# Kernel tuning notes

Measured on AMD Instinct MI355X. Metric: run time of the kernel, lower is better.

## Reference

```python
import jax, jax.numpy as jnp
import numpy as np

DIM = 1024
D_STATE = 16
D_CONV = 4
EXPAND = 2
D_INNER = DIM * EXPAND
DT_RANK = 64  # ceil(1024/16)
N_EXP = 8
TOP_K = 2
HID = DIM * 2
B, T = 2, 2048
EPS = 1e-5


def setup_inputs() -> dict:
    key = jax.random.key(0)
    ks = jax.random.split(key, 16)
    s = 0.02
    # dt bias init (softplus-inverse of dt in [1e-3, 1e-1]) as in the torch code
    dt_init = jnp.exp(jax.random.uniform(ks[0], (D_INNER,)) * (np.log(0.1) - np.log(0.001)) + np.log(0.001))
    dt_proj_b = dt_init + jnp.log(-jnp.expm1(-dt_init))
    A_log = jnp.broadcast_to(jnp.log(jnp.arange(1, D_STATE + 1, dtype=jnp.float32))[None, :], (D_INNER, D_STATE))
    return {
        "x": jax.random.normal(ks[1], (B, T, DIM), jnp.float32),
        "ssm_state": jnp.zeros((B, D_INNER, D_STATE), jnp.float32),
        "conv_state": jnp.zeros((B, D_INNER, D_CONV - 1), jnp.float32),
        "ln1_s": jnp.ones((DIM,), jnp.float32), "ln1_b": jnp.zeros((DIM,), jnp.float32),
        "ln2_s": jnp.ones((DIM,), jnp.float32), "ln2_b": jnp.zeros((DIM,), jnp.float32),
        "in_proj_w": jax.random.normal(ks[2], (2 * D_INNER, DIM), jnp.float32) * s,
        "conv_w": jax.random.normal(ks[3], (D_INNER, 1, D_CONV), jnp.float32) * 0.2,
        "conv_b": jnp.zeros((D_INNER,), jnp.float32),
        "x_proj_w": jax.random.normal(ks[4], (DT_RANK + 2 * D_STATE, D_INNER), jnp.float32) * s,
        "dt_proj_w": jax.random.normal(ks[5], (D_INNER, DT_RANK), jnp.float32) * s,
        "dt_proj_b": dt_proj_b,
        "A_log": A_log,
        "Dp": jnp.ones((D_INNER,), jnp.float32),
        "out_proj_w": jax.random.normal(ks[6], (DIM, D_INNER), jnp.float32) * s,
        "router_w": jax.random.normal(ks[7], (N_EXP, DIM), jnp.float32) * s,
        "w_gate": jax.random.normal(ks[8], (N_EXP, HID, DIM), jnp.float32) * s,
        "w_up": jax.random.normal(ks[9], (N_EXP, HID, DIM), jnp.float32) * s,
        "w_down": jax.random.normal(ks[10], (N_EXP, DIM, HID), jnp.float32) * s,
    }


def _layernorm(x, scale, bias):
    mu = x.mean(-1, keepdims=True)
    var = ((x - mu) ** 2).mean(-1, keepdims=True)
    return (x - mu) * jax.lax.rsqrt(var + EPS) * scale + bias


def _mamba(xn, ssm_state, conv_state, in_proj_w, conv_w, conv_b, x_proj_w, dt_proj_w, dt_proj_b, A_log, Dp, out_proj_w):
    xz = jnp.einsum("btd,ed->bte", xn, in_proj_w)          # [B,T,2*di]
    x_in, z = xz[..., :D_INNER], xz[..., D_INNER:]
    # causal depthwise conv with running buffer
    xc = jnp.concatenate([conv_state, x_in.transpose(0, 2, 1)], axis=2)  # [B,di,T+dc-1]
    new_conv_state = xc[:, :, -(D_CONV - 1):]
    conv = jax.lax.conv_general_dilated(xc, conv_w, (1,), "VALID",
                                        dimension_numbers=("NCH", "OIH", "NCH"),
                                        feature_group_count=D_INNER)
    conv = conv + conv_b[None, :, None]
    xcs = jax.nn.silu(conv).transpose(0, 2, 1)              # [B,T,di]
    proj = jnp.einsum("bti,pi->btp", xcs, x_proj_w)
    dt_raw = proj[..., :DT_RANK]
    Bp = proj[..., DT_RANK:DT_RANK + D_STATE]
    Cp = proj[..., DT_RANK + D_STATE:]
    dt = jax.nn.softplus(jnp.einsum("btr,ir->bti", dt_raw, dt_proj_w) + dt_proj_b)
    A = -jnp.exp(A_log)                                     # [di,ds]

    def step(h, inp):
        dt_t, B_t, C_t, x_t = inp                           # [B,di],[B,ds],[B,ds],[B,di]
        dA = jnp.exp(dt_t[..., None] * A)                   # [B,di,ds]
        dB = dt_t[..., None] * B_t[:, None, :]
        h = dA * h + dB * x_t[..., None]
        y = jnp.sum(h * C_t[:, None, :], -1) + Dp * x_t
        return h, y

    xs = (dt.transpose(1, 0, 2), Bp.transpose(1, 0, 2), Cp.transpose(1, 0, 2), xcs.transpose(1, 0, 2))
    h, ys = jax.lax.scan(step, ssm_state, xs)
    y = ys.transpose(1, 0, 2) * jax.nn.silu(z)
    out = jnp.einsum("bti,di->btd", y, out_proj_w)
    return out, h, new_conv_state


def _moe(x, router_w, w_gate, w_up, w_down):
    Bb, Tt, D = x.shape
    xf = x.reshape(-1, D)                                   # [N,D]
    probs = jax.nn.softmax(xf @ router_w.T, axis=-1)        # [N,E]
    tw, ti = jax.lax.top_k(probs, TOP_K)
    tw = tw / tw.sum(-1, keepdims=True)
    gate = jax.nn.silu(jnp.einsum("nd,ehd->neh", xf, w_gate))
    up = jnp.einsum("nd,ehd->neh", xf, w_up)
    eo = jnp.einsum("neh,edh->ned", gate * up, w_down)      # [N,E,D]
    sel = jnp.take_along_axis(eo, ti[:, :, None], axis=1)   # [N,K,D]
    out = (tw[..., None] * sel).sum(1)
    return out.reshape(Bb, Tt, D)


def reference(x, ssm_state, conv_state, ln1_s, ln1_b, ln2_s, ln2_b, in_proj_w, conv_w, conv_b,
              x_proj_w, dt_proj_w, dt_proj_b, A_log, Dp, out_proj_w, router_w, w_gate, w_up, w_down):
    mamba_out, h, new_conv = _mamba(_layernorm(x, ln1_s, ln1_b), ssm_state, conv_state,
                                    in_proj_w, conv_w, conv_b, x_proj_w, dt_proj_w, dt_proj_b,
                                    A_log, Dp, out_proj_w)
    x1 = x + mamba_out
    out = x1 + _moe(_layernorm(x1, ln2_s, ln2_b), router_w, w_gate, w_up, w_down)
    return out
```

## Files before the change

kernel.cpp:

```cpp
#include <hip/hip_runtime.h>
#include <hip/hip_bf16.h>
#include <math.h>

#define DIM 1024
#define D_STATE 16
#define D_CONV 4
#define D_INNER 2048
#define DT_RANK 64
#define N_EXP 8
#define TOP_K 2
#define HID 2048
#define BB 2
#define TT 2048
#define NTOK (BB*TT)
#define NSLOT (NTOK*TOP_K)
#define EPS 1e-5f
#define NCHUNK 64
#define CLEN (TT/NCHUNK)
#define XPJ_KS 8
#define XPJ_KLEN (D_INNER/XPJ_KS)

#define OFF_R0   ((size_t)0)
#define OFF_R1   ((size_t)4194304)
#define OFF_R2   ((size_t)8388608)
#define OFF_XZ   ((size_t)10485760)
#define OFF_H    OFF_XZ
#define OFF_WU   ((size_t)18874368)
#define OFF_XCS  ((size_t)27262976)
#define OFF_DTP  ((size_t)35651584)
#define OFF_X1   ((size_t)44040192)
#define OFF_PROJ ((size_t)48234496)
#define OFF_TW   ((size_t)48627712)
#define OFF_INT  ((size_t)48635904)
#define OFF_XPW  ((size_t)48668672)
#define IO_TI    0
#define IO_CNT   8192
#define IO_CUR   8200
#define IO_OFS   8208
#define IO_TOK   8216
#define IO_SLOT  16408

typedef __attribute__((ext_vector_type(4))) float f32x4;
typedef __attribute__((ext_vector_type(8))) __bf16 bf16x8;
typedef __attribute__((ext_vector_type(4))) __bf16 bf16x4;

__device__ __forceinline__ float siluf(float v){ return v / (1.f + expf(-v)); }

__device__ __forceinline__ f32x4 mfma16(bf16x8 a, bf16x8 b, f32x4 c){
    return __builtin_amdgcn_mfma_f32_16x16x32_bf16(a, b, c, 0, 0, 0);
}

__device__ __forceinline__ void gload16(const void* g, void* l){
    __builtin_amdgcn_global_load_lds(
        (const __attribute__((address_space(1))) unsigned int*)g,
        (__attribute__((address_space(3))) unsigned int*)l, 16, 0, 0);
}

__device__ __forceinline__ void cvt_store16(__bf16* dst, f32x4 a0, f32x4 a1, f32x4 a2, f32x4 a3){
    bf16x8 p0, p1;
    #pragma unroll
    for (int j = 0; j < 4; ++j){
        p0[j]   = (__bf16)a0[j];
        p0[j+4] = (__bf16)a1[j];
        p1[j]   = (__bf16)a2[j];
        p1[j+4] = (__bf16)a3[j];
    }
    *(bf16x8*)dst = p0;
    *(bf16x8*)(dst+8) = p1;
}

__global__ __launch_bounds__(256) void cvt_w_kernel(const float* __restrict__ src,
    __bf16* __restrict__ dst, int n4)
{
    int i = blockIdx.x*256 + threadIdx.x;
    int stride = gridDim.x*256;
    for (; i < n4; i += stride){
        f32x4 v = *(const f32x4*)(src + (size_t)i*4);
        bf16x4 o;
        o[0] = (__bf16)v[0]; o[1] = (__bf16)v[1];
        o[2] = (__bf16)v[2]; o[3] = (__bf16)v[3];
        *(bf16x4*)(dst + (size_t)i*4) = o;
    }
}

__global__ __launch_bounds__(256) void cvt_pad_xproj(const float* __restrict__ src,
    __bf16* __restrict__ dst)
{
    int i = blockIdx.x*256 + threadIdx.x;
    int base = i*4;
    int row = base >> 11;
    bf16x4 o;
    if (row < 96){
        f32x4 v = *(const f32x4*)(src + base);
        o[0] = (__bf16)v[0]; o[1] = (__bf16)v[1];
        o[2] = (__bf16)v[2]; o[3] = (__bf16)v[3];
    } else {
        o[0] = (__bf16)0.f; o[1] = (__bf16)0.f;
        o[2] = (__bf16)0.f; o[3] = (__bf16)0.f;
    }
    *(bf16x4*)(dst + base) = o;
}

__global__ __launch_bounds__(256) void ln_kernel(const float* __restrict__ x,
    const float* __restrict__ s, const float* __restrict__ b,
    __bf16* __restrict__ obf)
{
    int t = blockIdx.x;
    const float* xp = x + (size_t)t * DIM;
    float v[4]; float sum = 0.f, sq = 0.f;
    #pragma unroll
    for (int j = 0; j < 4; ++j){
        v[j] = xp[threadIdx.x + 256*j];
        sum += v[j]; sq += v[j]*v[j];
    }
    #pragma unroll
    for (int off = 32; off; off >>= 1){
        sum += __shfl_xor(sum, off, 64);
        sq  += __shfl_xor(sq , off, 64);
    }
    __shared__ float red[4][2];
    int w = threadIdx.x >> 6, lane = threadIdx.x & 63;
    if (lane == 0){ red[w][0] = sum; red[w][1] = sq; }
    __syncthreads();
    sum = red[0][0]+red[1][0]+red[2][0]+red[3][0];
    sq  = red[0][1]+red[1][1]+red[2][1]+red[3][1];
    float mu = sum * (1.f/DIM);
    float var = sq * (1.f/DIM) - mu*mu;
    float r = rsqrtf(var + EPS);
    #pragma unroll
    for (int j = 0; j < 4; ++j){
        int d = threadIdx.x + 256*j;
        obf[(size_t)t*DIM + d] = (__bf16)((v[j]-mu)*r*s[d] + b[d]);
    }
}

__global__ __launch_bounds__(256) void ln2_router_kernel(const float* __restrict__ x,
    const float* __restrict__ s, const float* __restrict__ b,
    const float* __restrict__ rw, __bf16* __restrict__ obf,
    float* __restrict__ tw, int* __restrict__ ti, int* __restrict__ counts)
{
    int t = blockIdx.x;
    const float* xp = x + (size_t)t * DIM;
    float v[4]; float sum = 0.f, sq = 0.f;
    #pragma unroll
    for (int j = 0; j < 4; ++j){
        v[j] = xp[threadIdx.x + 256*j];
        sum += v[j]; sq += v[j]*v[j];
    }
    #pragma unroll
    for (int off = 32; off; off >>= 1){
        sum += __shfl_xor(sum, off, 64);
        sq  += __shfl_xor(sq , off, 64);
    }
    __shared__ float red[4][2];
    __shared__ float red2[4][N_EXP];
    int w = threadIdx.x >> 6, lane = threadIdx.x & 63;
    if (lane == 0){ red[w][0] = sum; red[w][1] = sq; }
    __syncthreads();
    sum = red[0][0]+red[1][0]+red[2][0]+red[3][0];
    sq  = red[0][1]+red[1][1]+red[2][1]+red[3][1];
    float mu = sum * (1.f/DIM);
    float var = sq * (1.f/DIM) - mu*mu;
    float r = rsqrtf(var + EPS);
    float p[N_EXP] = {};
    #pragma unroll
    for (int j = 0; j < 4; ++j){
        int d = threadIdx.x + 256*j;
        float o = (v[j]-mu)*r*s[d] + b[d];
        obf[(size_t)t*DIM + d] = (__bf16)o;
        #pragma unroll
        for (int e = 0; e < N_EXP; ++e) p[e] += o * rw[e*DIM + d];
    }
    #pragma unroll
    for (int e = 0; e < N_EXP; ++e){
        #pragma unroll
        for (int off = 32; off; off >>= 1) p[e] += __shfl_xor(p[e], off, 64);
    }
    if (lane == 0){
        #pragma unroll
        for (int e = 0; e < N_EXP; ++e) red2[w][e] = p[e];
    }
    __syncthreads();
    if (threadIdx.x == 0){
        float q[N_EXP];
        #pragma unroll
        for (int e = 0; e < N_EXP; ++e)
            q[e] = red2[0][e]+red2[1][e]+red2[2][e]+red2[3][e];
        float mx = q[0];
        #pragma unroll
        for (int e = 1; e < N_EXP; ++e) mx = fmaxf(mx, q[e]);
        float ssum = 0.f;
        #pragma unroll
        for (int e = 0; e < N_EXP; ++e){ q[e] = expf(q[e]-mx); ssum += q[e]; }
        int i0 = 0;
        #pragma unroll
        for (int e = 1; e < N_EXP; ++e) if (q[e] > q[i0]) i0 = e;
        int i1 = (i0 == 0) ? 1 : 0;
        #pragma unroll
        for (int e = 0; e < N_EXP; ++e) if (e != i0 && q[e] > q[i1]) i1 = e;
        float w0 = q[i0]/ssum, w1 = q[i1]/ssum;
        float sw = w0 + w1; w0 /= sw; w1 /= sw;
        tw[t*2] = w0; tw[t*2+1] = w1;
        ti[t*2] = i0; ti[t*2+1] = i1;
        atomicAdd(&counts[i0], 1);
        atomicAdd(&counts[i1], 1);
    }
}

template<int MODE, int EPI, int CBF, int SWZ>
__global__ __launch_bounds__(256,3) void mfma_gemm_fast(
    const __bf16* __restrict__ A, const __bf16* __restrict__ W,
    const void* __restrict__ RG, void* __restrict__ Cv,
    const int* __restrict__ tok_of_slot, const int* __restrict__ counts,
    const int* __restrict__ offs, int M, int N, int K, int lda)
{
    int bx = blockIdx.x, by = blockIdx.y;
    if (SWZ){
        int nwg = gridDim.x*gridDim.y;
        int id = by*gridDim.x + bx;
        int swz = (id & 7)*(nwg >> 3) + (id >> 3);
        bx = swz % gridDim.x; by = swz / gridDim.x;
    }
    int e    = (MODE == 0) ? 0 : blockIdx.z;
    int cnt  = (MODE == 0) ? M : counts[e];
    int base = (MODE == 0) ? 0 : offs[e];
    int m0 = by * 128;
    if (m0 >= cnt) return;
    int n0 = bx * 128;
    const __bf16* We = W + (size_t)e * N * K;

    __shared__ __bf16 As[2*128*32];
    __shared__ __bf16 Ws[2*128*32];

    int tid = threadIdx.x;
    int wave = tid >> 6, lane = tid & 63;
    int c0 = wave*2, c1 = wave*2 + 1;
    int lr0 = c0*16 + (lane >> 2);
    int lr1 = c1*16 + (lane >> 2);
    int koff = (((lane & 3) ^ ((lane >> 3) & 3)) * 8);

    int ar0, ar1;
    {
        int m0c = m0 + lr0, m1c = m0 + lr1;
        if (MODE != 0){
            if (m0c >= cnt) m0c = cnt - 1;
            if (m1c >= cnt) m1c = cnt - 1;
        }
        if (MODE == 1){ ar0 = tok_of_slot[base + m0c]; ar1 = tok_of_slot[base + m1c]; }
        else if (MODE == 2){ ar0 = base + m0c; ar1 = base + m1c; }
        else { ar0 = m0c; ar1 = m1c; }
    }
    const __bf16* aS0 = A + (size_t)ar0 * lda + koff;
    const __bf16* aS1 = A + (size_t)ar1 * lda + koff;
    const __bf16* wS0 = We + (size_t)(n0 + lr0) * K + koff;
    const __bf16* wS1 = We + (size_t)(n0 + lr1) * K + koff;
    __bf16* ldsA0 = As + c0*512;
    __bf16* ldsA1 = As + c1*512;
    __bf16* ldsW0 = Ws + c0*512;
    __bf16* ldsW1 = Ws + c1*512;

    int wm = (wave >> 1) * 64, wn = (wave & 1) * 64;
    int fr = lane & 15;
    const int scb = (((lane >> 4) ^ ((lane >> 1) & 3)) * 8);

    f32x4 acc[4][4];
    #pragma unroll
    for (int i = 0; i < 4; ++i)
        #pragma unroll
        for (int j = 0; j < 4; ++j)
            acc[i][j] = (f32x4){0.f, 0.f, 0.f, 0.f};

    gload16(aS0, ldsA0);
    gload16(aS1, ldsA1);
    gload16(wS0, ldsW0);
    gload16(wS1, ldsW1);

    int bo = 0;
    for (int k0 = 0; k0 < K; k0 += 32){
        int nbo = bo ^ 4096;
        if (k0 + 32 < K){
            gload16(aS0 + k0 + 32, ldsA0 + nbo);
            gload16(aS1 + k0 + 32, ldsA1 + nbo);
            gload16(wS0 + k0 + 32, ldsW0 + nbo);
            gload16(wS1 + k0 + 32, ldsW1 + nbo);
            asm volatile("s_waitcnt vmcnt(4)" ::: "memory");
        } else {
            asm volatile("s_waitcnt vmcnt(0)" ::: "memory");
        }
        __builtin_amdgcn_s_barrier();
        bf16x8 af[4], bf[4];
        #pragma unroll
        for (int i = 0; i < 4; ++i)
            af[i] = *(const bf16x8*)&As[bo + (wm + i*16 + fr)*32 + scb];
        #pragma unroll
        for (int j = 0; j < 4; ++j)
            bf[j] = *(const bf16x8*)&Ws[bo + (wn + j*16 + fr)*32 + scb];
        #pragma unroll
        for (int i = 0; i < 4; ++i)
            #pragma unroll
            for (int j = 0; j < 4; ++j)
                acc[i][j] = mfma16(af[i], bf[j], acc[i][j]);
        __builtin_amdgcn_s_barrier();
        bo = nbo;
    }

    int orow = (lane >> 4) * 4;
    int ocol = lane & 15;
    #pragma unroll
    for (int i = 0; i < 4; ++i){
        #pragma unroll
        for (int jj = 0; jj < 4; ++jj){
            #pragma unroll
            for (int j = 0; j < 4; ++j){
                int m = m0 + wm + i*16 + orow + j;
                int n = n0 + wn + jj*16 + ocol;
                if (m < cnt){
                    size_t row = (size_t)(base + m);
                    float v = acc[i][jj][j];
                    if (EPI == 1) v += ((const float*)RG)[row * (size_t)N + n];
                    if (CBF) ((__bf16*)Cv)[row * (size_t)N + n] = (__bf16)v;
                    else     ((float* )Cv)[row * (size_t)N + n] = v;
                }
            }
        }
    }
}

__global__ __launch_bounds__(256,2) void moe_gateup_fast(
    const __bf16* __restrict__ A, const __bf16* __restrict__ Wg,
    const __bf16* __restrict__ Wu, const int* __restrict__ tok_of_slot,
    const int* __restrict__ counts, const int* __restrict__ offs,
    __bf16* __restrict__ H)
{
    int e = blockIdx.z;
    int cnt = counts[e];
    int base = offs[e];
    int m0 = blockIdx.y * 128;
    if (m0 >= cnt) return;
    int n0 = blockIdx.x * 128;
    const __bf16* Wge = Wg + (size_t)e * HID * DIM;
    const __bf16* Wue = Wu + (size_t)e * HID * DIM;

    __shared__ __bf16 As[2*128*32];
    __shared__ __bf16 Gs[2*128*32];
    __shared__ __bf16 Us[2*128*32];

    int tid = threadIdx.x;
    int wave = tid >> 6, lane = tid & 63;
    int c0 = wave*2, c1 = wave*2 + 1;
    int lr0 = c0*16 + (lane >> 2);
    int lr1 = c1*16 + (lane >> 2);
    int koff = (((lane & 3) ^ ((lane >> 3) & 3)) * 8);

    int m0c = m0 + lr0, m1c = m0 + lr1;
    if (m0c >= cnt) m0c = cnt - 1;
    if (m1c >= cnt) m1c = cnt - 1;
    int ar0 = tok_of_slot[base + m0c];
    int ar1 = tok_of_slot[base + m1c];

    const __bf16* aS0 = A + (size_t)ar0 * DIM + koff;
    const __bf16* aS1 = A + (size_t)ar1 * DIM + koff;
    const __bf16* gS0 = Wge + (size_t)(n0 + lr0) * DIM + koff;
    const __bf16* gS1 = Wge + (size_t)(n0 + lr1) * DIM + koff;
    const __bf16* uS0 = Wue + (size_t)(n0 + lr0) * DIM + koff;
    const __bf16* uS1 = Wue + (size_t)(n0 + lr1) * DIM + koff;
    __bf16* ldsA0 = As + c0*512;
    __bf16* ldsA1 = As + c1*512;
    __bf16* ldsG0 = Gs + c0*512;
    __bf16* ldsG1 = Gs + c1*512;
    __bf16* ldsU0 = Us + c0*512;
    __bf16* ldsU1 = Us + c1*512;

    int wm = (wave >> 1) * 64, wn = (wave & 1) * 64;
    int fr = lane & 15;
    const int scb = (((lane >> 4) ^ ((lane >> 1) & 3)) * 8);

    f32x4 accg[4][4], accu[4][4];
    #pragma unroll
    for (int i = 0; i < 4; ++i)
        #pragma unroll
        for (int j = 0; j < 4; ++j){
            accg[i][j] = (f32x4){0.f, 0.f, 0.f, 0.f};
            accu[i][j] = (f32x4){0.f, 0.f, 0.f, 0.f};
        }

    gload16(aS0, ldsA0);
    gload16(aS1, ldsA1);
    gload16(gS0, ldsG0);
    gload16(gS1, ldsG1);
    gload16(uS0, ldsU0);
    gload16(uS1, ldsU1);

    int bo = 0;
    for (int k0 = 0; k0 < DIM; k0 += 32){
        int nbo = bo ^ 4096;
        if (k0 + 32 < DIM){
            gload16(aS0 + k0 + 32, ldsA0 + nbo);
            gload16(aS1 + k0 + 32, ldsA1 + nbo);
            gload16(gS0 + k0 + 32, ldsG0 + nbo);
            gload16(gS1 + k0 + 32, ldsG1 + nbo);
            gload16(uS0 + k0 + 32, ldsU0 + nbo);
            gload16(uS1 + k0 + 32, ldsU1 + nbo);
            asm volatile("s_waitcnt vmcnt(6)" ::: "memory");
        } else {
            asm volatile("s_waitcnt vmcnt(0)" ::: "memory");
        }
        __builtin_amdgcn_s_barrier();
        bf16x8 af[4], gf[4], uf[4];
        #pragma unroll
        for (int i = 0; i < 4; ++i){
            af[i] = *(const bf16x8*)&As[bo + (wm + i*16 + fr)*32 + scb];
            gf[i] = *(const bf16x8*)&Gs[bo + (wn + i*16 + fr)*32 + scb];
            uf[i] = *(const bf16x8*)&Us[bo + (wn + i*16 + fr)*32 + scb];
        }
        #pragma unroll
        for (int i = 0; i < 4; ++i)
            #pragma unroll
            for (int j = 0; j < 4; ++j){
                accg[i][j] = mfma16(af[i], gf[j], accg[i][j]);
                accu[i][j] = mfma16(af[i], uf[j], accu[i][j]);
            }
        __builtin_amdgcn_s_barrier();
        bo = nbo;
    }

    int orow = (lane >> 4) * 4;
    int ocol = lane & 15;
    #pragma unroll
    for (int i = 0; i < 4; ++i){
        #pragma unroll
        for (int jj = 0; jj < 4; ++jj){
            #pragma unroll
            for (int j = 0; j < 4; ++j){
                int m = m0 + wm + i*16 + orow + j;
                if (m < cnt){
                    int n = n0 + wn + jj*16 + ocol;
                    size_t row = (size_t)(base + m);
                    float g = accg[i][jj][j], u = accu[i][jj][j];
                    H[row * (size_t)HID + n] = (__bf16)(siluf(g) * u);
                }
            }
        }
    }
}

__global__ __launch_bounds__(256,3) void xproj_ks_kernel(
    const __bf16* __restrict__ A, const __bf16* __restrict__ W,
    float* __restrict__ Cpart)
{
    int m0 = blockIdx.y * 128;
    int kbeg = blockIdx.z * XPJ_KLEN;

    __shared__ __bf16 As[2*128*32];
    __shared__ __bf16 Ws[2*128*32];

    int tid = threadIdx.x;
    int wave = tid >> 6, lane = tid & 63;
    int c0 = wave*2, c1 = wave*2 + 1;
    int lr0 = c0*16 + (lane >> 2);
    int lr1 = c1*16 + (lane >> 2);
    int koff = (((lane & 3) ^ ((lane >> 3) & 3)) * 8);

    const __bf16* aS0 = A + (size_t)(m0 + lr0) * D_INNER + kbeg + koff;
    const __bf16* aS1 = A + (size_t)(m0 + lr1) * D_INNER + kbeg + koff;
    const __bf16* wS0 = W + (size_t)lr0 * D_INNER + kbeg + koff;
    const __bf16* wS1 = W + (size_t)lr1 * D_INNER + kbeg + koff;
    __bf16* ldsA0 = As + c0*512;
    __bf16* ldsA1 = As + c1*512;
    __bf16* ldsW0 = Ws + c0*512;
    __bf16* ldsW1 = Ws + c1*512;

    int wm = (wave >> 1) * 64, wn = (wave & 1) * 64;
    int fr = lane & 15;
    const int scb = (((lane >> 4) ^ ((lane >> 1) & 3)) * 8);

    f32x4 acc[4][4];
    #pragma unroll
    for (int i = 0; i < 4; ++i)
        #pragma unroll
        for (int j = 0; j < 4; ++j)
            acc[i][j] = (f32x4){0.f, 0.f, 0.f, 0.f};

    gload16(aS0, ldsA0);
    gload16(aS1, ldsA1);
    gload16(wS0, ldsW0);
    gload16(wS1, ldsW1);

    int bo = 0;
    for (int k0 = 0; k0 < XPJ_KLEN; k0 += 32){
        int nbo = bo ^ 4096;
        if (k0 + 32 < XPJ_KLEN){
            gload16(aS0 + k0 + 32, ldsA0 + nbo);
            gload16(aS1 + k0 + 32, ldsA1 + nbo);
            gload16(wS0 + k0 + 32, ldsW0 + nbo);
            gload16(wS1 + k0 + 32, ldsW1 + nbo);
            asm volatile("s_waitcnt vmcnt(4)" ::: "memory");
        } else {
            asm volatile("s_waitcnt vmcnt(0)" ::: "memory");
        }
        __builtin_amdgcn_s_barrier();
        bf16x8 af[4], bf[4];
        #pragma unroll
        for (int i = 0; i < 4; ++i)
            af[i] = *(const bf16x8*)&As[bo + (wm + i*16 + fr)*32 + scb];
        #pragma unroll
        for (int j = 0; j < 4; ++j)
            bf[j] = *(const bf16x8*)&Ws[bo + (wn + j*16 + fr)*32 + scb];
        #pragma unroll
        for (int i = 0; i < 4; ++i)
            #pragma unroll
            for (int j = 0; j < 4; ++j)
                acc[i][j] = mfma16(af[i], bf[j], acc[i][j]);
        __builtin_amdgcn_s_barrier();
        bo = nbo;
    }

    float* Cz = Cpart + (size_t)blockIdx.z * NTOK * 128;
    int orow = (lane >> 4) * 4;
    int ocol = lane & 15;
    #pragma unroll
    for (int i = 0; i < 4; ++i){
        #pragma unroll
        for (int jj = 0; jj < 4; ++jj){
            #pragma unroll
            for (int j = 0; j < 4; ++j){
                int m = m0 + wm + i*16 + orow + j;
                int n = wn + jj*16 + ocol;
                Cz[(size_t)m * 128 + n] = acc[i][jj][j];
            }
        }
    }
}

__global__ __launch_bounds__(256) void xproj_reduce(const float* __restrict__ Cpart,
    float* __restrict__ proj)
{
    int idx = blockIdx.x*256 + threadIdx.x;
    int t = idx / 96, n = idx - t*96;
    float s = 0.f;
    #pragma unroll
    for (int z = 0; z < XPJ_KS; ++z)
        s += Cpart[(size_t)z * NTOK * 128 + (size_t)t * 128 + n];
    proj[idx] = s;
}

__global__ __launch_bounds__(256,2) void dt_gemm(
    const float* __restrict__ A, const float* __restrict__ W,
    const float* __restrict__ bias, float* __restrict__ C,
    int M, int N, int K, int lda)
{
    int m0 = blockIdx.y * 128;
    int n0 = blockIdx.x * 128;

    __shared__ __bf16 As[128*32];
    __shared__ __bf16 Ws[128*32];

    int tid = threadIdx.x;
    int srow = tid >> 1;
    int scol = (tid & 1) * 16;

    const float* af = A + (size_t)(m0 + srow) * lda + scol;
    const float* wptr = W + (size_t)(n0 + srow) * K + scol;

    f32x4 raf[4], rw[4];
    #pragma unroll
    for (int q = 0; q < 4; ++q){
        raf[q] = *(const f32x4*)(af + q*4);
        rw[q]  = *(const f32x4*)(wptr + q*4);
    }

    int wave = tid >> 6, lane = tid & 63;
    int wm = (wave >> 1) * 64, wn = (wave & 1) * 64;
    int fr = lane & 15, fk = (lane >> 4) * 8;

    f32x4 acc[4][4];
    #pragma unroll
    for (int i = 0; i < 4; ++i)
        #pragma unroll
        for (int j = 0; j < 4; ++j)
            acc[i][j] = (f32x4){0.f, 0.f, 0.f, 0.f};

    for (int k0 = 0; k0 < K; k0 += 32){
        cvt_store16(&As[srow*32 + scol], raf[0], raf[1], raf[2], raf[3]);
        cvt_store16(&Ws[srow*32 + scol], rw[0], rw[1], rw[2], rw[3]);
        __syncthreads();
        if (k0 + 32 < K){
            #pragma unroll
            for (int q = 0; q < 4; ++q){
                raf[q] = *(const f32x4*)(af + k0 + 32 + q*4);
                rw[q]  = *(const f32x4*)(wptr + k0 + 32 + q*4);
            }
        }
        bf16x8 afr[4], bfr[4];
        #pragma unroll
        for (int i = 0; i < 4; ++i)
            afr[i] = *(const bf16x8*)&As[(wm + i*16 + fr)*32 + fk];
        #pragma unroll
        for (int i = 0; i < 4; ++i)
            bfr[i] = *(const bf16x8*)&Ws[(wn + i*16 + fr)*32 + fk];
        #pragma unroll
        for (int i = 0; i < 4; ++i)
            #pragma unroll
            for (int j = 0; j < 4; ++j)
                acc[i][j] = mfma16(afr[i], bfr[j], acc[i][j]);
        __syncthreads();
    }

    int orow = (lane >> 4) * 4;
    int ocol = lane & 15;
    #pragma unroll
    for (int i = 0; i < 4; ++i){
        #pragma unroll
        for (int jj = 0; jj < 4; ++jj){
            #pragma unroll
            for (int j = 0; j < 4; ++j){
                int m = m0 + wm + i*16 + orow + j;
                int n = n0 + wn + jj*16 + ocol;
                if (m < M && n < N){
                    float v = acc[i][jj][j] + bias[n];
                    v = (v > 20.f) ? v : log1pf(expf(v));
                    C[(size_t)m * N + n] = v;
                }
            }
        }
    }
}

__global__ __launch_bounds__(256) void conv_kernel(const float* __restrict__ xz,
    const float* __restrict__ cs, const float* __restrict__ cw,
    const float* __restrict__ cb, float* __restrict__ xcs,
    __bf16* __restrict__ xcs_bf)
{
    int idx = blockIdx.x*256 + threadIdx.x;
    int d = idx & (D_INNER-1);
    int bt = idx >> 11;
    int b = bt >> 11;
    int t = bt & (TT-1);
    float acc = cb[d];
    #pragma unroll
    for (int k = 0; k < 4; ++k){
        int tau = t + k - 3;
        float xv;
        if (tau >= 0) xv = xz[(size_t)(b*TT + tau)*(2*D_INNER) + d];
        else          xv = cs[((size_t)b*D_INNER + d)*3 + (tau + 3)];
        acc += cw[d*4 + k] * xv;
    }
    float v = siluf(acc);
    xcs[idx] = v;
    xcs_bf[idx] = (__bf16)v;
}

__global__ __launch_bounds__(256) void scan_pass1(const float* __restrict__ dtp,
    const float* __restrict__ proj, const float* __restrict__ xcs,
    const float* __restrict__ A_log, float* __restrict__ hend,
    float* __restrict__ sumdt)
{
    int gid = blockIdx.x*256 + threadIdx.x;
    int bd = gid & (BB*D_INNER-1);
    int chunk = gid >> 12;
    int b = bd >> 11, d = bd & (D_INNER-1);
    float As[D_STATE], h[D_STATE];
    #pragma unroll
    for (int s = 0; s < D_STATE; ++s){
        As[s] = -__expf(A_log[d*D_STATE + s]);
        h[s] = 0.f;
    }
    float sdt = 0.f;
    int base = b*TT + chunk*CLEN;
    for (int t = 0; t < CLEN; ++t){
        size_t bt = (size_t)(base + t);
        float dt = dtp[bt*D_INNER + d];
        float x  = xcs[bt*D_INNER + d];
        f32x4 Bv[4];
        #pragma unroll
        for (int q = 0; q < 4; ++q) Bv[q] = *(const f32x4*)(proj + bt*96 + DT_RANK + q*4);
        float dtx = dt * x;
        sdt += dt;
        #pragma unroll
        for (int s = 0; s < D_STATE; ++s)
            h[s] = __expf(dt*As[s])*h[s] + Bv[s>>2][s&3]*dtx;
    }
    size_t hb = ((size_t)bd*NCHUNK + chunk)*D_STATE;
    #pragma unroll
    for (int q = 0; q < 4; ++q)
        *(f32x4*)(hend + hb + q*4) = (f32x4){h[q*4], h[q*4+1], h[q*4+2], h[q*4+3]};
    sumdt[bd*NCHUNK + chunk] = sdt;
}

__global__ __launch_bounds__(256) void scan_combine(const float* __restrict__ hend,
    const float* __restrict__ sumdt, const float* __restrict__ A_log,
    const float* __restrict__ ssm0, float* __restrict__ hstart)
{
    int gid = blockIdx.x*256 + threadIdx.x;
    int s = gid & 15;
    int bd = gid >> 4;
    int b = bd >> 11, d = bd & (D_INNER-1);
    float As = -__expf(A_log[d*D_STATE + s]);
    float h = ssm0[((size_t)b*D_INNER + d)*D_STATE + s];
    for (int c = 0; c < NCHUNK; ++c){
        size_t idx = ((size_t)bd*NCHUNK + c)*D_STATE + s;
        hstart[idx] = h;
        h = hend[idx] + __expf(As * sumdt[bd*NCHUNK + c]) * h;
    }
}

__global__ __launch_bounds__(256) void scan_pass3(const float* __restrict__ dtp,
    const float* __restrict__ proj, const float* __restrict__ xcs,
    const float* __restrict__ xz, const float* __restrict__ A_log,
    const float* __restrict__ Dp, const float* __restrict__ hstart,
    __bf16* __restrict__ ym)
{
    int gid = blockIdx.x*256 + threadIdx.x;
    int bd = gid & (BB*D_INNER-1);
    int chunk = gid >> 12;
    int b = bd >> 11, d = bd & (D_INNER-1);
    float As[D_STATE], h[D_STATE];
    #pragma unroll
    for (int s = 0; s < D_STATE; ++s)
        As[s] = -__expf(A_log[d*D_STATE + s]);
    size_t hb = ((size_t)bd*NCHUNK + chunk)*D_STATE;
    #pragma unroll
    for (int q = 0; q < 4; ++q){
        f32x4 hv = *(const f32x4*)(hstart + hb + q*4);
        h[q*4] = hv[0]; h[q*4+1] = hv[1]; h[q*4+2] = hv[2]; h[q*4+3] = hv[3];
    }
    float Dd = Dp[d];
    int base = b*TT + chunk*CLEN;
    for (int t = 0; t < CLEN; ++t){
        size_t bt = (size_t)(base + t);
        float dt = dtp[bt*D_INNER + d];
        float x  = xcs[bt*D_INNER + d];
        f32x4 Bv[4], Cv[4];
        #pragma unroll
        for (int q = 0; q < 4; ++q){
            Bv[q] = *(const f32x4*)(proj + bt*96 + DT_RANK + q*4);
            Cv[q] = *(const f32x4*)(proj + bt*96 + DT_RANK + D_STATE + q*4);
        }
        float dtx = dt * x;
        float p = 0.f;
        #pragma unroll
        for (int s = 0; s < D_STATE; ++s){
            h[s] = __expf(dt*As[s])*h[s] + Bv[s>>2][s&3]*dtx;
            p += h[s] * Cv[s>>2][s&3];
        }
        float y = p + Dd*x;
        float z = xz[bt*(2*D_INNER) + D_INNER + d];
        float sz = z / (1.f + __expf(-z));
        ym[bt*D_INNER + d] = (__bf16)(y * sz);
    }
}

__global__ void offs_kernel(const int* __restrict__ counts, int* __restrict__ offs)
{
    if (threadIdx.x == 0 && blockIdx.x == 0){
        int s = 0;
        for (int e = 0; e < N_EXP; ++e){ offs[e] = s; s += counts[e]; }
    }
}

__global__ __launch_bounds__(256) void assign_kernel(const int* __restrict__ ti,
    const int* __restrict__ offs, int* __restrict__ cursors,
    int* __restrict__ tok_of_slot, int* __restrict__ slot_of)
{
    int t = blockIdx.x*256 + threadIdx.x;
    if (t >= NTOK) return;
    #pragma unroll
    for (int k = 0; k < TOP_K; ++k){
        int e = ti[t*2 + k];
        int pos = atomicAdd(&cursors[e], 1);
        int slot = offs[e] + pos;
        tok_of_slot[slot] = t;
        slot_of[t*2 + k] = slot;
    }
}

__global__ __launch_bounds__(256) void final_kernel(const float* __restrict__ x1,
    const float* __restrict__ down_out, const float* __restrict__ tw,
    const int* __restrict__ slot_of, float* __restrict__ out)
{
    int idx4 = blockIdx.x*256 + threadIdx.x;
    int t = idx4 >> 8;
    int c = idx4 & 255;
    float w0 = tw[t*2], w1 = tw[t*2+1];
    size_t s0 = (size_t)slot_of[t*2] * DIM;
    size_t s1 = (size_t)slot_of[t*2+1] * DIM;
    float4 a = *(const float4*)(x1 + (size_t)t*DIM + c*4);
    float4 d0 = *(const float4*)(down_out + s0 + c*4);
    float4 d1 = *(const float4*)(down_out + s1 + c*4);
    float4 r;
    r.x = a.x + w0*d0.x + w1*d1.x;
    r.y = a.y + w0*d0.y + w1*d1.y;
    r.z = a.z + w0*d0.z + w1*d1.z;
    r.w = a.w + w0*d0.w + w1*d1.w;
    *(float4*)(out + (size_t)t*DIM + c*4) = r;
}

extern "C" void kernel_launch(void* const* d_in, const int* in_sizes, int n_in,
                              void* d_out, int out_size, void* d_ws, size_t ws_size,
                              hipStream_t stream)
{
    const float* x        = (const float*)d_in[0];
    const float* ssm0     = (const float*)d_in[1];
    const float* conv0    = (const float*)d_in[2];
    const float* ln1_s    = (const float*)d_in[3];
    const float* ln1_b    = (const float*)d_in[4];
    const float* ln2_s    = (const float*)d_in[5];
    const float* ln2_b    = (const float*)d_in[6];
    const float* in_proj  = (const float*)d_in[7];
    const float* conv_w   = (const float*)d_in[8];
    const float* conv_b   = (const float*)d_in[9];
    const float* x_proj   = (const float*)d_in[10];
    const float* dt_proj  = (const float*)d_in[11];
    const float* dt_b     = (const float*)d_in[12];
    const float* A_log    = (const float*)d_in[13];
    const float* Dp       = (const float*)d_in[14];
    const float* out_proj = (const float*)d_in[15];
    const float* router_w = (const float*)d_in[16];
    const float* w_gate   = (const float*)d_in[17];
    const float* w_up     = (const float*)d_in[18];
    const float* w_down   = (const float*)d_in[19];
    float* out = (float*)d_out;

    float* ws = (float*)d_ws;
    __bf16* xn_bf  = (__bf16*)(ws + OFF_R0);
    float*  hend   = ws + OFF_R0;
    __bf16* ym_bf  = (__bf16*)(ws + OFF_R0);
    float*  xpart  = ws + OFF_R1;
    float*  hst    = ws + OFF_R1;
    float*  sdt    = ws + OFF_R2;
    __bf16* opbf   = (__bf16*)(ws + OFF_R2);
    __bf16* xn2bf  = (__bf16*)(ws + OFF_R2);
    float*  xz     = ws + OFF_XZ;
    __bf16* H      = (__bf16*)(ws + OFF_H);
    __bf16* wubf   = (__bf16*)(ws + OFF_WU);
    float*  xcs    = ws + OFF_XCS;
    float*  dnout  = ws + OFF_XCS;
    float*  dtp    = ws + OFF_DTP;
    __bf16* ipbf   = (__bf16*)(ws + OFF_DTP);
    __bf16* wgbf   = (__bf16*)(ws + OFF_DTP);
    __bf16* wdbf   = (__bf16*)(ws + OFF_DTP);
    __bf16* xcs_bf = (__bf16*)(ws + OFF_X1);
    float*  x1     = ws + OFF_X1;
    float*  proj   = ws + OFF_PROJ;
    float*  tw     = ws + OFF_TW;
    __bf16* xpw    = (__bf16*)(ws + OFF_XPW);
    int*    ip     = (int*)(ws + OFF_INT);
    int* ti          = ip + IO_TI;
    int* counts      = ip + IO_CNT;
    int* cursors     = ip + IO_CUR;
    int* offs        = ip + IO_OFS;
    int* tok_of_slot = ip + IO_TOK;
    int* slot_of     = ip + IO_SLOT;

    hipMemsetAsync(counts, 0, 16*sizeof(int), stream);

    cvt_w_kernel<<<1024, 256, 0, stream>>>(in_proj, ipbf, (2*D_INNER*DIM)/4);
    ln_kernel<<<NTOK, 256, 0, stream>>>(x, ln1_s, ln1_b, xn_bf);
    mfma_gemm_fast<0,0,0,1><<<dim3(32,32), 256, 0, stream>>>(xn_bf, ipbf, nullptr, xz,
        nullptr, nullptr, nullptr, NTOK, 2*D_INNER, DIM, DIM);
    conv_kernel<<<(NTOK*D_INNER)/256, 256, 0, stream>>>(xz, conv0, conv_w, conv_b, xcs, xcs_bf);
    cvt_pad_xproj<<<256, 256, 0, stream>>>(x_proj, xpw);
    xproj_ks_kernel<<<dim3(1,32,XPJ_KS), 256, 0, stream>>>(xcs_bf, xpw, xpart);
    xproj_reduce<<<(NTOK*96)/256, 256, 0, stream>>>(xpart, proj);
    dt_gemm<<<dim3(16,32), 256, 0, stream>>>(proj, dt_proj, dt_b, dtp,
        NTOK, D_INNER, DT_RANK, 96);
    scan_pass1<<<1024, 256, 0, stream>>>(dtp, proj, xcs, A_log, hend, sdt);
    scan_combine<<<256, 256, 0, stream>>>(hend, sdt, A_log, ssm0, hst);
    scan_pass3<<<1024, 256, 0, stream>>>(dtp, proj, xcs, xz, A_log, Dp, hst, ym_bf);
    cvt_w_kernel<<<512, 256, 0, stream>>>(out_proj, opbf, (DIM*D_INNER)/4);
    mfma_gemm_fast<0,1,0,1><<<dim3(8,32), 256, 0, stream>>>(ym_bf, opbf, x, x1,
        nullptr, nullptr, nullptr, NTOK, DIM, D_INNER, D_INNER);
    ln2_router_kernel<<<NTOK, 256, 0, stream>>>(x1, ln2_s, ln2_b, router_w,
        xn2bf, tw, ti, counts);
    offs_kernel<<<1, 64, 0, stream>>>(counts, offs);
    assign_kernel<<<NTOK/256, 256, 0, stream>>>(ti, offs, cursors, tok_of_slot, slot_of);
    cvt_w_kernel<<<2048, 256, 0, stream>>>(w_gate, wgbf, (N_EXP*HID*DIM)/4);
    cvt_w_kernel<<<2048, 256, 0, stream>>>(w_up, wubf, (N_EXP*HID*DIM)/4);
    moe_gateup_fast<<<dim3(HID/128, 64, N_EXP), 256, 0, stream>>>(xn2bf, wgbf, wubf,
        tok_of_slot, counts, offs, H);
    cvt_w_kernel<<<2048, 256, 0, stream>>>(w_down, wdbf, (N_EXP*DIM*HID)/4);
    mfma_gemm_fast<2,0,0,0><<<dim3(DIM/128, 64, N_EXP), 256, 0, stream>>>(H, wdbf, nullptr, dnout,
        tok_of_slot, counts, offs, NSLOT, DIM, HID, HID);
    final_kernel<<<(NTOK*DIM/4)/256, 256, 0, stream>>>(x1, dnout, tw, slot_of, out);
}
```

Before: 740.0 us.

## Triple-buffer LDS in GEMM kernels and raise wave priority around MFMA

Converts the generic GEMM, the MoE gate/up GEMM and the x_proj split-K GEMM from a double-buffered to a triple-buffered LDS pipeline, prefetching two K-steps ahead with adjusted vmcnt waits. It also wraps the MFMA block in s_setprio so compute waves get scheduling priority. The aim is to hide global-load latency better, at the cost of more LDS per block (the gate/up kernel grows to 72KB), which may lower occupancy.

```diff
diff --git a/kernel.cpp b/kernel.cpp
--- a/kernel.cpp
+++ b/kernel.cpp
@@ -229,8 +229,8 @@
     int n0 = bx * 128;
     const __bf16* We = W + (size_t)e * N * K;
 
-    __shared__ __bf16 As[2*128*32];
-    __shared__ __bf16 Ws[2*128*32];
+    __shared__ __bf16 As[3*128*32];
+    __shared__ __bf16 Ws[3*128*32];
 
     int tid = threadIdx.x;
     int wave = tid >> 6, lane = tid & 63;
@@ -270,24 +270,32 @@
         for (int j = 0; j < 4; ++j)
             acc[i][j] = (f32x4){0.f, 0.f, 0.f, 0.f};
 
-    gload16(aS0, ldsA0);
-    gload16(aS1, ldsA1);
-    gload16(wS0, ldsW0);
-    gload16(wS1, ldsW1);
-
-    int bo = 0;
-    for (int k0 = 0; k0 < K; k0 += 32){
-        int nbo = bo ^ 4096;
-        if (k0 + 32 < K){
-            gload16(aS0 + k0 + 32, ldsA0 + nbo);
-            gload16(aS1 + k0 + 32, ldsA1 + nbo);
-            gload16(wS0 + k0 + 32, ldsW0 + nbo);
-            gload16(wS1 + k0 + 32, ldsW1 + nbo);
+    int NK = K >> 5;
+    gload16(aS0, ldsA0);        gload16(aS1, ldsA1);
+    gload16(wS0, ldsW0);        gload16(wS1, ldsW1);
+    if (NK > 1){
+        gload16(aS0 + 32, ldsA0 + 4096); gload16(aS1 + 32, ldsA1 + 4096);
+        gload16(wS0 + 32, ldsW0 + 4096); gload16(wS1 + 32, ldsW1 + 4096);
+    }
+
+    int cur = 0;
+    for (int t = 0; t < NK; ++t){
+        if (t + 2 < NK){
+            int nb = cur + 2; if (nb >= 3) nb -= 3;
+            int off = nb*4096;
+            size_t ko = (size_t)(t+2)*32;
+            gload16(aS0 + ko, ldsA0 + off);
+            gload16(aS1 + ko, ldsA1 + off);
+            gload16(wS0 + ko, ldsW0 + off);
+            gload16(wS1 + ko, ldsW1 + off);
+            asm volatile("s_waitcnt vmcnt(8)" ::: "memory");
+        } else if (t + 1 < NK){
             asm volatile("s_waitcnt vmcnt(4)" ::: "memory");
         } else {
             asm volatile("s_waitcnt vmcnt(0)" ::: "memory");
         }
         __builtin_amdgcn_s_barrier();
+        int bo = cur*4096;
         bf16x8 af[4], bf[4];
         #pragma unroll
         for (int i = 0; i < 4; ++i)
@@ -295,13 +303,15 @@
         #pragma unroll
         for (int j = 0; j < 4; ++j)
             bf[j] = *(const bf16x8*)&Ws[bo + (wn + j*16 + fr)*32 + scb];
+        __builtin_amdgcn_s_setprio(1);
         #pragma unroll
         for (int i = 0; i < 4; ++i)
             #pragma unroll
             for (int j = 0; j < 4; ++j)
                 acc[i][j] = mfma16(af[i], bf[j], acc[i][j]);
+        __builtin_amdgcn_s_setprio(0);
         __builtin_amdgcn_s_barrier();
-        bo = nbo;
+        cur = cur + 1; if (cur >= 3) cur -= 3;
     }
 
     int orow = (lane >> 4) * 4;
@@ -341,9 +351,9 @@
     const __bf16* Wge = Wg + (size_t)e * HID * DIM;
     const __bf16* Wue = Wu + (size_t)e * HID * DIM;
 
-    __shared__ __bf16 As[2*128*32];
-    __shared__ __bf16 Gs[2*128*32];
-    __shared__ __bf16 Us[2*128*32];
+    __shared__ __bf16 As[3*128*32];
+    __shared__ __bf16 Gs[3*128*32];
+    __shared__ __bf16 Us[3*128*32];
 
     int tid = threadIdx.x;
     int wave = tid >> 6, lane = tid & 63;
@@ -384,28 +394,34 @@
             accu[i][j] = (f32x4){0.f, 0.f, 0.f, 0.f};
         }
 
-    gload16(aS0, ldsA0);
-    gload16(aS1, ldsA1);
-    gload16(gS0, ldsG0);
-    gload16(gS1, ldsG1);
-    gload16(uS0, ldsU0);
-    gload16(uS1, ldsU1);
-
-    int bo = 0;
-    for (int k0 = 0; k0 < DIM; k0 += 32){
-        int nbo = bo ^ 4096;
-        if (k0 + 32 < DIM){
-            gload16(aS0 + k0 + 32, ldsA0 + nbo);
-            gload16(aS1 + k0 + 32, ldsA1 + nbo);
-            gload16(gS0 + k0 + 32, ldsG0 + nbo);
-            gload16(gS1 + k0 + 32, ldsG1 + nbo);
-            gload16(uS0 + k0 + 32, ldsU0 + nbo);
-            gload16(uS1 + k0 + 32, ldsU1 + nbo);
+    gload16(aS0, ldsA0); gload16(aS1, ldsA1);
+    gload16(gS0, ldsG0); gload16(gS1, ldsG1);
+    gload16(uS0, ldsU0); gload16(uS1, ldsU1);
+    gload16(aS0 + 32, ldsA0 + 4096); gload16(aS1 + 32, ldsA1 + 4096);
+    gload16(gS0 + 32, ldsG0 + 4096); gload16(gS1 + 32, ldsG1 + 4096);
+    gload16(uS0 + 32, ldsU0 + 4096); gload16(uS1 + 32, ldsU1 + 4096);
+
+    const int NK = DIM >> 5;
+    int cur = 0;
+    for (int t = 0; t < NK; ++t){
+        if (t + 2 < NK){
+            int nb = cur + 2; if (nb >= 3) nb -= 3;
+            int off = nb*4096;
+            size_t ko = (size_t)(t+2)*32;
+            gload16(aS0 + ko, ldsA0 + off);
+            gload16(aS1 + ko, ldsA1 + off);
+            gload16(gS0 + ko, ldsG0 + off);
+            gload16(gS1 + ko, ldsG1 + off);
+            gload16(uS0 + ko, ldsU0 + off);
+            gload16(uS1 + ko, ldsU1 + off);
+            asm volatile("s_waitcnt vmcnt(12)" ::: "memory");
+        } else if (t + 1 < NK){
             asm volatile("s_waitcnt vmcnt(6)" ::: "memory");
         } else {
             asm volatile("s_waitcnt vmcnt(0)" ::: "memory");
         }
         __builtin_amdgcn_s_barrier();
+        int bo = cur*4096;
         bf16x8 af[4], gf[4], uf[4];
         #pragma unroll
         for (int i = 0; i < 4; ++i){
@@ -413,6 +429,7 @@
             gf[i] = *(const bf16x8*)&Gs[bo + (wn + i*16 + fr)*32 + scb];
             uf[i] = *(const bf16x8*)&Us[bo + (wn + i*16 + fr)*32 + scb];
         }
+        __builtin_amdgcn_s_setprio(1);
         #pragma unroll
         for (int i = 0; i < 4; ++i)
             #pragma unroll
@@ -420,8 +437,9 @@
                 accg[i][j] = mfma16(af[i], gf[j], accg[i][j]);
                 accu[i][j] = mfma16(af[i], uf[j], accu[i][j]);
             }
+        __builtin_amdgcn_s_setprio(0);
         __builtin_amdgcn_s_barrier();
-        bo = nbo;
+        cur = cur + 1; if (cur >= 3) cur -= 3;
     }
 
     int orow = (lane >> 4) * 4;
@@ -451,8 +469,8 @@
     int m0 = blockIdx.y * 128;
     int kbeg = blockIdx.z * XPJ_KLEN;
 
-    __shared__ __bf16 As[2*128*32];
-    __shared__ __bf16 Ws[2*128*32];
+    __shared__ __bf16 As[3*128*32];
+    __shared__ __bf16 Ws[3*128*32];
 
     int tid = threadIdx.x;
     int wave = tid >> 6, lane = tid & 63;
@@ -481,24 +499,30 @@
         for (int j = 0; j < 4; ++j)
             acc[i][j] = (f32x4){0.f, 0.f, 0.f, 0.f};
 
-    gload16(aS0, ldsA0);
-    gload16(aS1, ldsA1);
-    gload16(wS0, ldsW0);
-    gload16(wS1, ldsW1);
-
-    int bo = 0;
-    for (int k0 = 0; k0 < XPJ_KLEN; k0 += 32){
-        int nbo = bo ^ 4096;
-        if (k0 + 32 < XPJ_KLEN){
-            gload16(aS0 + k0 + 32, ldsA0 + nbo);
-            gload16(aS1 + k0 + 32, ldsA1 + nbo);
-            gload16(wS0 + k0 + 32, ldsW0 + nbo);
-            gload16(wS1 + k0 + 32, ldsW1 + nbo);
+    gload16(aS0, ldsA0); gload16(aS1, ldsA1);
+    gload16(wS0, ldsW0); gload16(wS1, ldsW1);
+    gload16(aS0 + 32, ldsA0 + 4096); gload16(aS1 + 32, ldsA1 + 4096);
+    gload16(wS0 + 32, ldsW0 + 4096); gload16(wS1 + 32, ldsW1 + 4096);
+
+    const int NK = XPJ_KLEN >> 5;
+    int cur = 0;
+    for (int t = 0; t < NK; ++t){
+        if (t + 2 < NK){
+            int nb = cur + 2; if (nb >= 3) nb -= 3;
+            int off = nb*4096;
+            size_t ko = (size_t)(t+2)*32;
+            gload16(aS0 + ko, ldsA0 + off);
+            gload16(aS1 + ko, ldsA1 + off);
+            gload16(wS0 + ko, ldsW0 + off);
+            gload16(wS1 + ko, ldsW1 + off);
+            asm volatile("s_waitcnt vmcnt(8)" ::: "memory");
+        } else if (t + 1 < NK){
             asm volatile("s_waitcnt vmcnt(4)" ::: "memory");
         } else {
             asm volatile("s_waitcnt vmcnt(0)" ::: "memory");
         }
         __builtin_amdgcn_s_barrier();
+        int bo = cur*4096;
         bf16x8 af[4], bf[4];
         #pragma unroll
         for (int i = 0; i < 4; ++i)
@@ -506,13 +530,15 @@
         #pragma unroll
         for (int j = 0; j < 4; ++j)
             bf[j] = *(const bf16x8*)&Ws[bo + (wn + j*16 + fr)*32 + scb];
+        __builtin_amdgcn_s_setprio(1);
         #pragma unroll
         for (int i = 0; i < 4; ++i)
             #pragma unroll
             for (int j = 0; j < 4; ++j)
                 acc[i][j] = mfma16(af[i], bf[j], acc[i][j]);
+        __builtin_amdgcn_s_setprio(0);
         __builtin_amdgcn_s_barrier();
-        bo = nbo;
+        cur = cur + 1; if (cur >= 3) cur -= 3;
     }
 
     float* Cz = Cpart + (size_t)blockIdx.z * NTOK * 128;
```

New measurement: 738.5 us. No clear change (-0.2%).
